# Kernel tuning notes

Measured on AMD Instinct MI355X. Metric: run time of the kernel, lower is better.

The kernel has to match this reference:

```python
import jax, jax.numpy as jnp
import numpy as np
import math

B, N, D = 4, 2048, 512
H, DH = 8, 128
INNER = H * DH


def setup_inputs() -> dict:
    key = jax.random.key(0)
    k1, k2, k3, k4 = jax.random.split(key, 4)
    x = jax.random.normal(k1, (B, N, D), dtype=jnp.float32)
    Wg = jax.random.normal(k2, (D, INNER), dtype=jnp.float32) * (1.0 / math.sqrt(D))
    Wout = jax.random.normal(k3, (INNER, D), dtype=jnp.float32) * (1.0 / math.sqrt(INNER))
    sigma = jax.random.uniform(k4, (1, H, 1, 1), dtype=jnp.float32, minval=0.5, maxval=2.5)
    return {"x": x, "Wg": Wg, "Wout": Wout, "sigma": sigma}


def reference(x, Wg, Wout, sigma):
    b, n, d = x.shape
    h, dh = H, DH
    # value projection: [b,n,d] @ [d, h*dh] -> [b,h,n,dh]
    v = (x @ Wg).reshape(b, n, h, dh).transpose(0, 2, 1, 3)
    # fixed Gaussian positional mask, shared across batch: build once per head
    pos = jnp.arange(1, n + 1, dtype=jnp.float32)
    diffs = jnp.abs(pos[:, None] - pos[None, :])  # [n, n]
    sig = sigma.reshape(h, 1, 1)  # [h,1,1]
    inv_norm = 1.0 / (jnp.sqrt(2.0 * jnp.float32(math.pi)) * sig)
    gauss = inv_norm * jnp.exp(-(diffs[None] ** 2) / (2.0 * sig ** 2))  # [h,n,n]
    corr = gauss / gauss.sum(-1, keepdims=True)  # row-normalized [h,n,n]
    # attention: broadcast mask over batch
    attn = jnp.einsum('hnm,bhmd->bhnd', corr, v)
    out = attn.transpose(0, 2, 1, 3).reshape(b, n, h * dh)
    return out @ Wout  # dropout p=0.0 -> identity
```

## Files before the change

kernel.cpp:

```cpp
#include <hip/hip_runtime.h>
#include <hip/hip_bf16.h>
#include <math.h>

#define B_ 4
#define N_ 2048
#define D_ 512
#define H_ 8
#define DH_ 128
#define INNER_ 1024
#define W_ 32
#define M_ (B_ * N_)

typedef __attribute__((ext_vector_type(8))) short short8;
typedef __attribute__((ext_vector_type(4))) float floatx4;

typedef const __attribute__((address_space(1))) char* gcp;
typedef __attribute__((address_space(3))) char* lcp;

__device__ __forceinline__ float bf16hi_to_f(unsigned u) {
    union { unsigned u; float f; } c; c.u = u; return c.f;
}

template <typename OutT>
__global__ __launch_bounds__(256, 4) void gemm_bf16_mfma64(
    const __hip_bfloat16* __restrict__ A, const __hip_bfloat16* __restrict__ Bt,
    OutT* __restrict__ C, int M, int N, int K)
{
    __shared__ __hip_bfloat16 Asm[64 * 64];
    __shared__ __hip_bfloat16 Bsm[64 * 64];

    const int tid  = threadIdx.x;
    const int lane = tid & 63;
    const int w    = tid >> 6;
    const int wm   = w >> 1;
    const int wn   = w & 1;
    const int bm   = blockIdx.y;
    const int bn   = blockIdx.x;

    const int kh = lane >> 4;
    const int ml = lane & 15;

    floatx4 acc[2][2];
    #pragma unroll
    for (int i = 0; i < 2; ++i)
        #pragma unroll
        for (int j = 0; j < 2; ++j) acc[i][j] = (floatx4){0.f, 0.f, 0.f, 0.f};

    const char* Ab = (const char*)(A + (size_t)(bm * 64) * K);
    const char* Bb = (const char*)(Bt + (size_t)(bn * 64) * K);
    const size_t rowstride = (size_t)K * 2;

    for (int k0 = 0; k0 < K; k0 += 64) {
        #pragma unroll
        for (int it = 0; it < 2; ++it) {
            int o = it * 4096 + tid * 16;
            int r = o >> 7;
            int s = (o >> 4) & 7;
            int c = s ^ (r & 7);
            size_t goff = (size_t)r * rowstride + (size_t)k0 * 2 + c * 16;
            __builtin_amdgcn_global_load_lds((gcp)(Ab + goff), (lcp)((char*)Asm + o), 16, 0, 0);
            __builtin_amdgcn_global_load_lds((gcp)(Bb + goff), (lcp)((char*)Bsm + o), 16, 0, 0);
        }
        __syncthreads();

        const short* As = (const short*)Asm;
        const short* Bs = (const short*)Bsm;
        short8 af[2][2], bf[2][2];
        #pragma unroll
        for (int t = 0; t < 2; ++t) {
            int ra = wm * 32 + t * 16 + ml;
            int rb = wn * 32 + t * 16 + ml;
            #pragma unroll
            for (int kk = 0; kk < 2; ++kk) {
                int ch = kk * 4 + kh;
                af[t][kk] = *(const short8*)(As + ra * 64 + ((ch ^ (ra & 7)) * 8));
                bf[t][kk] = *(const short8*)(Bs + rb * 64 + ((ch ^ (rb & 7)) * 8));
            }
        }
        #pragma unroll
        for (int kk = 0; kk < 2; ++kk)
            #pragma unroll
            for (int i = 0; i < 2; ++i)
                #pragma unroll
                for (int j = 0; j < 2; ++j)
                    acc[i][j] = __builtin_amdgcn_mfma_f32_16x16x32_bf16(
                        af[i][kk], bf[j][kk], acc[i][j], 0, 0, 0);
        __syncthreads();
    }

    const int rq = lane >> 4;
    const int cl = lane & 15;
    #pragma unroll
    for (int i = 0; i < 2; ++i) {
        #pragma unroll
        for (int j = 0; j < 2; ++j) {
            #pragma unroll
            for (int r = 0; r < 4; ++r) {
                int row = bm * 64 + wm * 32 + i * 16 + rq * 4 + r;
                int col = bn * 64 + wn * 32 + j * 16 + cl;
                if constexpr (sizeof(OutT) == 2)
                    C[(size_t)row * N + col] = __float2bfloat16(acc[i][j][r]);
                else
                    C[(size_t)row * N + col] = acc[i][j][r];
            }
        }
    }
}

__global__ __launch_bounds__(256) void cast_bf16(
    const float* __restrict__ src, __hip_bfloat16* __restrict__ dst, int n8)
{
    int i = blockIdx.x * 256 + threadIdx.x;
    if (i >= n8) return;
    const float4* s = (const float4*)src + i * 2;
    float4 a = s[0], b = s[1];
    __hip_bfloat16 o[8] = {
        __float2bfloat16(a.x), __float2bfloat16(a.y), __float2bfloat16(a.z), __float2bfloat16(a.w),
        __float2bfloat16(b.x), __float2bfloat16(b.y), __float2bfloat16(b.z), __float2bfloat16(b.w)};
    *(short8*)(dst + (size_t)i * 8) = *(short8*)o;
}

__global__ __launch_bounds__(256) void transpose_cast(
    const float* __restrict__ src, __hip_bfloat16* __restrict__ dst, int R, int Cn)
{
    __shared__ float t[32][33];
    int c0 = blockIdx.x * 32, r0 = blockIdx.y * 32;
    int lx = threadIdx.x, ly = threadIdx.y;
    #pragma unroll
    for (int i = 0; i < 32; i += 8)
        t[ly + i][lx] = src[(size_t)(r0 + ly + i) * Cn + c0 + lx];
    __syncthreads();
    #pragma unroll
    for (int i = 0; i < 32; i += 8)
        dst[(size_t)(c0 + ly + i) * R + r0 + lx] = __float2bfloat16(t[lx][ly + i]);
}

#define TNA 64
#define ROWSB (TNA + 2 * W_)

struct bf16x4s { __hip_bfloat16 a, b, c, d; };

__global__ __launch_bounds__(256) void banded_attn2(
    const __hip_bfloat16* __restrict__ v, const float* __restrict__ sigma,
    __hip_bfloat16* __restrict__ attn)
{
    __shared__ __hip_bfloat16 vs[ROWSB][DH_];
    __shared__ float wtab[2 * W_ + 1];
    __shared__ float winv[TNA];

    const int tid = threadIdx.x;
    const int n0 = blockIdx.x * TNA;
    const int h  = blockIdx.y;
    const int b  = blockIdx.z;

    const __hip_bfloat16* vbase = v + (size_t)b * N_ * INNER_ + h * DH_;
    #pragma unroll
    for (int it = 0; it < 8; ++it) {
        int idx = tid + it * 256;
        int r = idx >> 4;
        int g = idx & 15;
        int m = n0 - W_ + r;
        int4 val = make_int4(0, 0, 0, 0);
        if (m >= 0 && m < N_) val = *(const int4*)(vbase + (size_t)m * INNER_ + g * 8);
        *(int4*)&vs[r][g * 8] = val;
    }
    if (tid <= 2 * W_) {
        float sig = sigma[h];
        float d = (float)(tid - W_);
        wtab[tid] = __expf(-d * d / (2.0f * sig * sig));
    }
    __syncthreads();

    if (tid < TNA) {
        int n = n0 + tid;
        float ws = 0.f;
        #pragma unroll
        for (int j = 0; j <= 2 * W_; ++j) {
            int m = n - W_ + j;
            ws += (m >= 0 && m < N_) ? wtab[j] : 0.f;
        }
        winv[tid] = 1.0f / ws;
    }
    __syncthreads();

    const int cg = tid & 31;
    const int rg = tid >> 5;

    float4 acc[8];
    #pragma unroll
    for (int r = 0; r < 8; ++r) acc[r] = make_float4(0.f, 0.f, 0.f, 0.f);
    float wreg[8] = {0.f, 0.f, 0.f, 0.f, 0.f, 0.f, 0.f, 0.f};

    const unsigned* vrow0 = (const unsigned*)&vs[rg * 8][cg * 4];

    #pragma unroll 8
    for (int l = 0; l < 2 * W_ + 8; ++l) {
        wreg[l & 7] = (l <= 2 * W_) ? wtab[l] : 0.f;
        const unsigned* p = vrow0 + (size_t)l * (DH_ / 2);
        unsigned r0 = p[0], r1 = p[1];
        float4 vv;
        vv.x = bf16hi_to_f(r0 << 16);
        vv.y = bf16hi_to_f(r0 & 0xffff0000u);
        vv.z = bf16hi_to_f(r1 << 16);
        vv.w = bf16hi_to_f(r1 & 0xffff0000u);
        #pragma unroll
        for (int r = 0; r < 8; ++r) {
            float wgt = wreg[(l - r) & 7];
            acc[r].x += wgt * vv.x; acc[r].y += wgt * vv.y;
            acc[r].z += wgt * vv.z; acc[r].w += wgt * vv.w;
        }
    }

    #pragma unroll
    for (int r = 0; r < 8; ++r) {
        int nl = rg * 8 + r;
        float s = winv[nl];
        bf16x4s o = { __float2bfloat16(acc[r].x * s), __float2bfloat16(acc[r].y * s),
                      __float2bfloat16(acc[r].z * s), __float2bfloat16(acc[r].w * s) };
        *(bf16x4s*)(attn + ((size_t)b * N_ + n0 + nl) * INNER_ + h * DH_ + cg * 4) = o;
    }
}

extern "C" void kernel_launch(void* const* d_in, const int* in_sizes, int n_in,
                              void* d_out, int out_size, void* d_ws, size_t ws_size,
                              hipStream_t stream) {
    const float* x     = (const float*)d_in[0];
    const float* Wg    = (const float*)d_in[1];
    const float* Wout  = (const float*)d_in[2];
    const float* sigma = (const float*)d_in[3];
    float* out = (float*)d_out;

    char* ws = (char*)d_ws;
    __hip_bfloat16* x_bf   = (__hip_bfloat16*)ws;
    __hip_bfloat16* Wg_t   = (__hip_bfloat16*)(ws + (((size_t)8)  << 20));
    __hip_bfloat16* Wout_t = (__hip_bfloat16*)(ws + (((size_t)9)  << 20));
    __hip_bfloat16* v_bf   = (__hip_bfloat16*)(ws + (((size_t)10) << 20));
    __hip_bfloat16* attn   = (__hip_bfloat16*)(ws + (((size_t)26) << 20));

    cast_bf16<<<dim3((M_ * D_ / 8 + 255) / 256), dim3(256), 0, stream>>>(x, x_bf, M_ * D_ / 8);
    transpose_cast<<<dim3(INNER_ / 32, D_ / 32), dim3(32, 8), 0, stream>>>(Wg, Wg_t, D_, INNER_);
    transpose_cast<<<dim3(D_ / 32, INNER_ / 32), dim3(32, 8), 0, stream>>>(Wout, Wout_t, INNER_, D_);

    gemm_bf16_mfma64<__hip_bfloat16><<<dim3(INNER_ / 64, M_ / 64), dim3(256), 0, stream>>>(
        x_bf, Wg_t, v_bf, M_, INNER_, D_);

    banded_attn2<<<dim3(N_ / TNA, H_, B_), dim3(256), 0, stream>>>(v_bf, sigma, attn);

    gemm_bf16_mfma64<float><<<dim3(D_ / 64, M_ / 64), dim3(256), 0, stream>>>(
        attn, Wout_t, out, M_, D_, INNER_);
}
```

Before: 137.3 us.

## Fuse prep kernels, stage GEMM epilogue through LDS, split banded attention channels

Merges the x cast and both weight transpose-casts into one prep launch, which cuts launch overhead. The GEMM epilogue now writes accumulators into shared memory and then stores coalesced 16-byte rows instead of scattered scalar stores. The banded attention kernel splits each head's 128 channels into two 64-channel blocks. That doubles the grid and lowers per-thread register use, at the cost of reloading the band halo and recomputing the weight tables twice as often.

```diff
diff --git a/kernel.cpp b/kernel.cpp
--- a/kernel.cpp
+++ b/kernel.cpp
@@ -26,8 +26,9 @@
     const __hip_bfloat16* __restrict__ A, const __hip_bfloat16* __restrict__ Bt,
     OutT* __restrict__ C, int M, int N, int K)
 {
-    __shared__ __hip_bfloat16 Asm[64 * 64];
-    __shared__ __hip_bfloat16 Bsm[64 * 64];
+    __shared__ char smem[16384];
+    __hip_bfloat16* Asm = (__hip_bfloat16*)smem;
+    __hip_bfloat16* Bsm = (__hip_bfloat16*)(smem + 8192);
 
     const int tid  = threadIdx.x;
     const int lane = tid & 63;
@@ -88,44 +89,51 @@
         __syncthreads();
     }
 
+    float* Cs = (float*)smem;
     const int rq = lane >> 4;
     const int cl = lane & 15;
     #pragma unroll
-    for (int i = 0; i < 2; ++i) {
-        #pragma unroll
-        for (int j = 0; j < 2; ++j) {
-            #pragma unroll
-            for (int r = 0; r < 4; ++r) {
-                int row = bm * 64 + wm * 32 + i * 16 + rq * 4 + r;
-                int col = bn * 64 + wn * 32 + j * 16 + cl;
-                if constexpr (sizeof(OutT) == 2)
-                    C[(size_t)row * N + col] = __float2bfloat16(acc[i][j][r]);
-                else
-                    C[(size_t)row * N + col] = acc[i][j][r];
-            }
-        }
-    }
-}
-
-__global__ __launch_bounds__(256) void cast_bf16(
-    const float* __restrict__ src, __hip_bfloat16* __restrict__ dst, int n8)
-{
-    int i = blockIdx.x * 256 + threadIdx.x;
-    if (i >= n8) return;
-    const float4* s = (const float4*)src + i * 2;
-    float4 a = s[0], b = s[1];
-    __hip_bfloat16 o[8] = {
-        __float2bfloat16(a.x), __float2bfloat16(a.y), __float2bfloat16(a.z), __float2bfloat16(a.w),
-        __float2bfloat16(b.x), __float2bfloat16(b.y), __float2bfloat16(b.z), __float2bfloat16(b.w)};
-    *(short8*)(dst + (size_t)i * 8) = *(short8*)o;
-}
-
-__global__ __launch_bounds__(256) void transpose_cast(
-    const float* __restrict__ src, __hip_bfloat16* __restrict__ dst, int R, int Cn)
+    for (int i = 0; i < 2; ++i)
+        #pragma unroll
+        for (int j = 0; j < 2; ++j)
+            #pragma unroll
+            for (int r = 0; r < 4; ++r)
+                Cs[(wm * 32 + i * 16 + rq * 4 + r) * 64 + wn * 32 + j * 16 + cl] = acc[i][j][r];
+    __syncthreads();
+
+    if constexpr (sizeof(OutT) == 2) {
+        int row = tid >> 3;
+        #pragma unroll
+        for (int p = 0; p < 2; ++p) {
+            int idx = p * 256 + tid;
+            int rr = idx >> 3;
+            int cc = (idx & 7) * 8;
+            const float* src = Cs + rr * 64 + cc;
+            __hip_bfloat16 o[8];
+            #pragma unroll
+            for (int e = 0; e < 8; ++e) o[e] = __float2bfloat16(src[e]);
+            *(short8*)((__hip_bfloat16*)C + (size_t)(bm * 64 + rr) * N + bn * 64 + cc) = *(short8*)o;
+        }
+        (void)row;
+    } else {
+        #pragma unroll
+        for (int p = 0; p < 4; ++p) {
+            int idx = p * 256 + tid;
+            int rr = idx >> 4;
+            int cc = (idx & 15) * 4;
+            float4 vv = *(const float4*)(Cs + rr * 64 + cc);
+            *(float4*)((float*)C + (size_t)(bm * 64 + rr) * N + bn * 64 + cc) = vv;
+        }
+    }
+}
+
+__device__ __forceinline__ void transpose32(
+    const float* __restrict__ src, __hip_bfloat16* __restrict__ dst,
+    int R, int Cn, int rt, int ct, int tid)
 {
     __shared__ float t[32][33];
-    int c0 = blockIdx.x * 32, r0 = blockIdx.y * 32;
-    int lx = threadIdx.x, ly = threadIdx.y;
+    int c0 = ct * 32, r0 = rt * 32;
+    int lx = tid & 31, ly = tid >> 5;
     #pragma unroll
     for (int i = 0; i < 32; i += 8)
         t[ly + i][lx] = src[(size_t)(r0 + ly + i) * Cn + c0 + lx];
@@ -135,30 +143,56 @@
         dst[(size_t)(c0 + ly + i) * R + r0 + lx] = __float2bfloat16(t[lx][ly + i]);
 }
 
+__global__ __launch_bounds__(256) void prep(
+    const float* __restrict__ x, const float* __restrict__ Wg,
+    const float* __restrict__ Wout, __hip_bfloat16* __restrict__ x_bf,
+    __hip_bfloat16* __restrict__ Wg_t, __hip_bfloat16* __restrict__ Wout_t)
+{
+    const int bid = blockIdx.x;
+    const int tid = threadIdx.x;
+    if (bid < 2048) {
+        int i = bid * 256 + tid;
+        const float4* s = (const float4*)x + (size_t)i * 2;
+        float4 a = s[0], b = s[1];
+        __hip_bfloat16 o[8] = {
+            __float2bfloat16(a.x), __float2bfloat16(a.y), __float2bfloat16(a.z), __float2bfloat16(a.w),
+            __float2bfloat16(b.x), __float2bfloat16(b.y), __float2bfloat16(b.z), __float2bfloat16(b.w)};
+        *(short8*)(x_bf + (size_t)i * 8) = *(short8*)o;
+    } else if (bid < 2560) {
+        int id2 = bid - 2048;
+        transpose32(Wg, Wg_t, D_, INNER_, id2 >> 5, id2 & 31, tid);
+    } else {
+        int id2 = bid - 2560;
+        transpose32(Wout, Wout_t, INNER_, D_, id2 >> 4, id2 & 15, tid);
+    }
+}
+
 #define TNA 64
 #define ROWSB (TNA + 2 * W_)
+#define CHB 64
 
 struct bf16x4s { __hip_bfloat16 a, b, c, d; };
 
-__global__ __launch_bounds__(256) void banded_attn2(
+__global__ __launch_bounds__(256) void banded_attn3(
     const __hip_bfloat16* __restrict__ v, const float* __restrict__ sigma,
     __hip_bfloat16* __restrict__ attn)
 {
-    __shared__ __hip_bfloat16 vs[ROWSB][DH_];
+    __shared__ __hip_bfloat16 vs[ROWSB][CHB];
     __shared__ float wtab[2 * W_ + 1];
     __shared__ float winv[TNA];
 
     const int tid = threadIdx.x;
-    const int n0 = blockIdx.x * TNA;
-    const int h  = blockIdx.y;
-    const int b  = blockIdx.z;
-
-    const __hip_bfloat16* vbase = v + (size_t)b * N_ * INNER_ + h * DH_;
-    #pragma unroll
-    for (int it = 0; it < 8; ++it) {
+    const int n0  = blockIdx.x * TNA;
+    const int h   = blockIdx.y >> 1;
+    const int ch0 = (blockIdx.y & 1) * CHB;
+    const int b   = blockIdx.z;
+
+    const __hip_bfloat16* vbase = v + (size_t)b * N_ * INNER_ + h * DH_ + ch0;
+    #pragma unroll
+    for (int it = 0; it < 4; ++it) {
         int idx = tid + it * 256;
-        int r = idx >> 4;
-        int g = idx & 15;
+        int r = idx >> 3;
+        int g = idx & 7;
         int m = n0 - W_ + r;
         int4 val = make_int4(0, 0, 0, 0);
         if (m >= 0 && m < N_) val = *(const int4*)(vbase + (size_t)m * INNER_ + g * 8);
@@ -183,20 +217,20 @@
     }
     __syncthreads();
 
-    const int cg = tid & 31;
-    const int rg = tid >> 5;
-
-    float4 acc[8];
-    #pragma unroll
-    for (int r = 0; r < 8; ++r) acc[r] = make_float4(0.f, 0.f, 0.f, 0.f);
-    float wreg[8] = {0.f, 0.f, 0.f, 0.f, 0.f, 0.f, 0.f, 0.f};
-
-    const unsigned* vrow0 = (const unsigned*)&vs[rg * 8][cg * 4];
-
-    #pragma unroll 8
-    for (int l = 0; l < 2 * W_ + 8; ++l) {
-        wreg[l & 7] = (l <= 2 * W_) ? wtab[l] : 0.f;
-        const unsigned* p = vrow0 + (size_t)l * (DH_ / 2);
+    const int cg = tid & 15;
+    const int rg = tid >> 4;
+
+    float4 acc[4];
+    #pragma unroll
+    for (int r = 0; r < 4; ++r) acc[r] = make_float4(0.f, 0.f, 0.f, 0.f);
+    float wreg[4] = {0.f, 0.f, 0.f, 0.f};
+
+    const unsigned* vrow0 = (const unsigned*)&vs[rg * 4][cg * 4];
+
+    #pragma unroll 4
+    for (int l = 0; l < 2 * W_ + 4; ++l) {
+        wreg[l & 3] = (l <= 2 * W_) ? wtab[l] : 0.f;
+        const unsigned* p = vrow0 + (size_t)l * (CHB / 2);
         unsigned r0 = p[0], r1 = p[1];
         float4 vv;
         vv.x = bf16hi_to_f(r0 << 16);
@@ -204,20 +238,20 @@
         vv.z = bf16hi_to_f(r1 << 16);
         vv.w = bf16hi_to_f(r1 & 0xffff0000u);
         #pragma unroll
-        for (int r = 0; r < 8; ++r) {
-            float wgt = wreg[(l - r) & 7];
+        for (int r = 0; r < 4; ++r) {
+            float wgt = wreg[(l - r) & 3];
             acc[r].x += wgt * vv.x; acc[r].y += wgt * vv.y;
             acc[r].z += wgt * vv.z; acc[r].w += wgt * vv.w;
         }
     }
 
     #pragma unroll
-    for (int r = 0; r < 8; ++r) {
-        int nl = rg * 8 + r;
+    for (int r = 0; r < 4; ++r) {
+        int nl = rg * 4 + r;
         float s = winv[nl];
         bf16x4s o = { __float2bfloat16(acc[r].x * s), __float2bfloat16(acc[r].y * s),
                       __float2bfloat16(acc[r].z * s), __float2bfloat16(acc[r].w * s) };
-        *(bf16x4s*)(attn + ((size_t)b * N_ + n0 + nl) * INNER_ + h * DH_ + cg * 4) = o;
+        *(bf16x4s*)(attn + ((size_t)b * N_ + n0 + nl) * INNER_ + h * DH_ + ch0 + cg * 4) = o;
     }
 }
 
@@ -237,14 +271,12 @@
     __hip_bfloat16* v_bf   = (__hip_bfloat16*)(ws + (((size_t)10) << 20));
     __hip_bfloat16* attn   = (__hip_bfloat16*)(ws + (((size_t)26) << 20));
 
-    cast_bf16<<<dim3((M_ * D_ / 8 + 255) / 256), dim3(256), 0, stream>>>(x, x_bf, M_ * D_ / 8);
-    transpose_cast<<<dim3(INNER_ / 32, D_ / 32), dim3(32, 8), 0, stream>>>(Wg, Wg_t, D_, INNER_);
-    transpose_cast<<<dim3(D_ / 32, INNER_ / 32), dim3(32, 8), 0, stream>>>(Wout, Wout_t, INNER_, D_);
+    prep<<<dim3(3072), dim3(256), 0, stream>>>(x, Wg, Wout, x_bf, Wg_t, Wout_t);
 
     gemm_bf16_mfma64<__hip_bfloat16><<<dim3(INNER_ / 64, M_ / 64), dim3(256), 0, stream>>>(
         x_bf, Wg_t, v_bf, M_, INNER_, D_);
 
-    banded_attn2<<<dim3(N_ / TNA, H_, B_), dim3(256), 0, stream>>>(v_bf, sigma, attn);
+    banded_attn3<<<dim3(N_ / TNA, H_ * 2, B_), dim3(256), 0, stream>>>(v_bf, sigma, attn);
 
     gemm_bf16_mfma64<float><<<dim3(D_ / 64, M_ / 64), dim3(256), 0, stream>>>(
         attn, Wout_t, out, M_, D_, INNER_);
```

Measured after the change: 137.0 us. No clear change (-0.3%).
